# Performance work log

Measured on AMD Instinct MI355X. Metric: run time of the kernel, lower is better.

The kernel has to match this reference:

```python
import jax, jax.numpy as jnp
import numpy as np

N, F, K, E = 50000, 128, 8, 1600000


def setup_inputs() -> dict:
    key = jax.random.key(0)
    k1, k2, k3, k4 = jax.random.split(key, 4)
    x = jax.random.normal(k1, (N, F), dtype=jnp.float32)
    adj = jax.random.randint(k2, (2, E), 0, N, dtype=jnp.int64)
    e = jax.random.normal(k3, (N, K), dtype=jnp.float32)
    stdv = 1.0 / np.sqrt(F)  # reset_parameters: uniform(-stdv, stdv)
    weights = jax.random.uniform(k4, (K, 2 * F, F), dtype=jnp.float32,
                                 minval=-stdv, maxval=stdv)
    return {"x": x, "adj": adj, "e": e, "weights": weights}


def _gcn_conv(x, row, col, n_nodes):
    # degree of each node as a message *destination* (col) -- matches torch degree(col, N)
    deg = jax.ops.segment_sum(jnp.ones(row.shape[0], x.dtype), col,
                              num_segments=n_nodes)
    val = (1.0 / jnp.sqrt(deg[col])) * (1.0 / jnp.sqrt(deg[row]))
    val = jnp.nan_to_num(val, nan=0.0, posinf=0.0, neginf=0.0)
    # SparseTensor(row=col, col=row) @ x : aggregate x[row] into col
    msg = val[:, None] * x[row]           # [E, F] gather
    return jax.ops.segment_sum(msg, col, num_segments=n_nodes)  # [N, F] scatter


def reference(x, adj, e, weights):
    n_nodes = x.shape[0]
    row, col = adj[0], adj[1]
    hi = _gcn_conv(x, row, col, n_nodes)                  # [N, F]
    hi = jnp.concatenate([hi, x], axis=1)                 # [N, 2F]
    # torch: repeat hi K times, bmm with [K,2F,F], transpose -> [N, K, F]
    outputs = jnp.einsum('nf,kfo->nko', hi, weights)      # [N, K, F]
    out = jnp.sum(e[:, :, None] * outputs, axis=1)        # gating sum over K
    out = out + x                                         # residual
    return out
```

## Files before the change

### kernel.cpp

```cpp
#include <hip/hip_runtime.h>
#include <hip/hip_bf16.h>

typedef __bf16 bf16_t;
typedef __bf16 bf16x8 __attribute__((ext_vector_type(8)));
typedef float f32x4 __attribute__((ext_vector_type(4)));
typedef float f32x2 __attribute__((ext_vector_type(2)));

#define F 128
#define KEXP 8
#define BM 256
#define SSTG 16384

#define NB 196
#define CAP 12288
#define CH 8192

__global__ __launch_bounds__(256) void k_binA(const int* __restrict__ row,
    const int* __restrict__ col, int* __restrict__ cursor,
    int* __restrict__ region, int E){
  __shared__ int stage[CH];
  __shared__ unsigned char stageb[CH];
  __shared__ int hist4[4][NB];
  __shared__ int lcur4[4][NB];
  int tid = threadIdx.x, wid = tid >> 6;
  int base = blockIdx.x * CH;
  int cnt = min(CH, E - base);
  for (int i = tid; i < 4*NB; i += 256) ((int*)hist4)[i] = 0;
  __syncthreads();
  for (int i = tid; i < cnt; i += 256){
    int r = row[base+i], c = col[base+i];
    stage[i] = (r << 8) | (c & 255);
    stageb[i] = (unsigned char)(c >> 8);
    atomicAdd(&hist4[wid][c >> 8], 1);
  }
  __syncthreads();
  for (int b = tid; b < NB; b += 256){
    int h0 = hist4[0][b], h1 = hist4[1][b], h2 = hist4[2][b], h3 = hist4[3][b];
    int gbase = atomicAdd(&cursor[b], h0+h1+h2+h3) + b*CAP;
    lcur4[0][b] = gbase;
    lcur4[1][b] = gbase + h0;
    lcur4[2][b] = gbase + h0 + h1;
    lcur4[3][b] = gbase + h0 + h1 + h2;
  }
  __syncthreads();
  for (int i = tid; i < cnt; i += 256){
    int b = stageb[i];
    int pos = atomicAdd(&lcur4[wid][b], 1);
    region[pos] = stage[i];
  }
}

__global__ void k_bstart(const int* __restrict__ cursor, int* __restrict__ bstart,
                         int* __restrict__ offs, int Nn){
  __shared__ int lds[256];
  int t = threadIdx.x;
  int c = (t < NB) ? cursor[t] : 0;
  lds[t] = c; __syncthreads();
  for (int off=1; off<256; off<<=1){
    int u = (t>=off) ? lds[t-off] : 0;
    __syncthreads();
    lds[t] += u;
    __syncthreads();
  }
  if (t < NB) bstart[t] = lds[t] - c;
  if (t == NB-1){ bstart[NB] = lds[t]; offs[Nn] = lds[t]; }
}

__global__ __launch_bounds__(256) void k_binB(const int* __restrict__ region,
    const int* __restrict__ cursor, const int* __restrict__ bstart,
    int* __restrict__ deg, int* __restrict__ offs, int* __restrict__ bucket,
    int Nn){
  __shared__ int hist4[4][256];
  __shared__ int loff[256];
  __shared__ int lcur4[4][256];
  int b = blockIdx.x, t = threadIdx.x, wid = t >> 6;
  int cnt = cursor[b];
  const int* src = region + b*CAP;
  for (int i = t; i < 4*256; i += 256) ((int*)hist4)[i] = 0;
  __syncthreads();
  for (int i = t; i < cnt; i += 256) atomicAdd(&hist4[wid][src[i] & 255], 1);
  __syncthreads();
  int h0 = hist4[0][t], h1 = hist4[1][t], h2 = hist4[2][t], h3 = hist4[3][t];
  int v = h0 + h1 + h2 + h3;
  loff[t] = v;
  __syncthreads();
  for (int off=1; off<256; off<<=1){
    int u = (t>=off) ? loff[t-off] : 0;
    __syncthreads();
    loff[t] += u;
    __syncthreads();
  }
  int excl = loff[t] - v;
  int gb = bstart[b];
  int node = b*256 + t;
  if (node < Nn){ deg[node] = v; offs[node] = gb + excl; }
  lcur4[0][t] = gb + excl;
  lcur4[1][t] = gb + excl + h0;
  lcur4[2][t] = gb + excl + h0 + h1;
  lcur4[3][t] = gb + excl + h0 + h1 + h2;
  __syncthreads();
  for (int i = t; i < cnt; i += 256){
    int p = src[i];
    int pos = atomicAdd(&lcur4[wid][p & 255], 1);
    bucket[pos] = p >> 8;
  }
}

__global__ void k_prep(const float* __restrict__ x, const int* __restrict__ deg,
                       unsigned int* __restrict__ xs8, const float* __restrict__ W,
                       bf16_t* __restrict__ Wt, int Nn, int xsB){
  int tid = threadIdx.x;
  if ((int)blockIdx.x < xsB){
    int i = blockIdx.x*256 + tid;
    if (i < Nn*16){
      int n = i >> 4;
      int d = deg[n];
      float dr = d>0 ? rsqrtf((float)d) : 0.f;
      const float4 f0 = *reinterpret_cast<const float4*>(&x[(size_t)i*8]);
      const float4 f1 = *reinterpret_cast<const float4*>(&x[(size_t)i*8+4]);
      unsigned int lo, hi2;
      lo  = __builtin_amdgcn_cvt_pk_fp8_f32(dr*f0.x, dr*f0.y, 0,  false);
      lo  = __builtin_amdgcn_cvt_pk_fp8_f32(dr*f0.z, dr*f0.w, lo, true);
      hi2 = __builtin_amdgcn_cvt_pk_fp8_f32(dr*f1.x, dr*f1.y, 0,  false);
      hi2 = __builtin_amdgcn_cvt_pk_fp8_f32(dr*f1.z, dr*f1.w, hi2, true);
      xs8[(size_t)i*2]     = lo;
      xs8[(size_t)i*2 + 1] = hi2;
    }
  } else {
    int i8 = (blockIdx.x - xsB)*256 + tid;
    if (i8 < 32768){
      int st   = i8 >> 11;
      int g    = i8 & 2047;
      int frag = g >> 6;
      int lane = g & 63;
      int h = st >> 3, kk = st & 7;
      int ksl = frag >> 3, cgg = frag & 7;
      int n  = cgg*16 + (lane & 15);
      int f0 = h*128 + ksl*32 + (lane >> 4)*8;
      bf16x8 v;
      #pragma unroll
      for (int j=0;j<8;j++)
        v[j] = (bf16_t)W[(size_t)kk*32768 + (size_t)(f0+j)*128 + n];
      *reinterpret_cast<bf16x8*>(&Wt[(size_t)i8*8]) = v;
    }
  }
}

__global__ __launch_bounds__(256) void k_agg(const unsigned int* __restrict__ xs8,
    const int* __restrict__ offs, const int* __restrict__ bucket,
    bf16_t* __restrict__ hi, int Nn){
  int wid = threadIdx.x >> 6, lane = threadIdx.x & 63;
  int g = lane >> 4, j16 = lane & 15;
  int n = blockIdx.x*16 + wid*4 + g;
  if (n >= Nn) return;
  int o0 = offs[n], o1 = offs[n+1];
  float acc[8] = {0.f,0.f,0.f,0.f,0.f,0.f,0.f,0.f};
  int nr = (o1 - o0 + 7) >> 3;
  int j = o0;
  for (int r = 0; r < nr; r++, j += 8){
    int idx[8];
    #pragma unroll
    for (int t=0;t<8;t++) idx[t] = bucket[min(j+t, o1-1)];
    uint2 v[8];
    #pragma unroll
    for (int t=0;t<8;t++)
      v[t] = *reinterpret_cast<const uint2*>(
          reinterpret_cast<const unsigned char*>(xs8) + (size_t)idx[t]*F + j16*8);
    #pragma unroll
    for (int t=0;t<8;t++){
      float m = (j+t < o1) ? 1.f : 0.f;
      f32x2 p0 = __builtin_amdgcn_cvt_pk_f32_fp8(v[t].x, false);
      f32x2 p1 = __builtin_amdgcn_cvt_pk_f32_fp8(v[t].x, true);
      f32x2 p2 = __builtin_amdgcn_cvt_pk_f32_fp8(v[t].y, false);
      f32x2 p3 = __builtin_amdgcn_cvt_pk_f32_fp8(v[t].y, true);
      acc[0] += m*p0.x; acc[1] += m*p0.y;
      acc[2] += m*p1.x; acc[3] += m*p1.y;
      acc[4] += m*p2.x; acc[5] += m*p2.y;
      acc[6] += m*p3.x; acc[7] += m*p3.y;
    }
  }
  int dn = o1 - o0;
  float dc = dn>0 ? rsqrtf((float)dn) : 0.f;
  bf16x8 o;
  #pragma unroll
  for (int i=0;i<8;i++) o[i] = (bf16_t)(dc*acc[i]);
  *reinterpret_cast<bf16x8*>(&hi[(size_t)n*F + j16*8]) = o;
}

#define MFMA_BF16 __builtin_amdgcn_mfma_f32_16x16x32_bf16

__global__ __launch_bounds__(512, 2) void k_gemm(
    const bf16_t* __restrict__ hi, const float* __restrict__ x,
    const float* __restrict__ e, const bf16_t* __restrict__ Wt,
    float* __restrict__ out, int Nn)
{
  extern __shared__ __align__(16) char smem[];
  bf16_t* b_s  = (bf16_t*)smem;
  float*  e_sT = (float*)(smem + 2*SSTG*2);
  const int tid = threadIdx.x;
  const int base = blockIdx.x * BM;
  const int lane = tid & 63, wid = tid >> 6;
  const int rw = wid >> 1, cw = wid & 1;
  const int r16 = lane & 15, kc = lane >> 4;

  #pragma unroll
  for (int i=0;i<4;i++){
    int u = tid + i*512;
    __builtin_amdgcn_global_load_lds(
        (const __attribute__((address_space(1))) void*)(Wt + (size_t)u*8),
        (__attribute__((address_space(3))) void*)(b_s + (size_t)u*8),
        16, 0, 0);
  }

  for (int i = tid; i < KEXP*BM; i += 512){
    int kk = i >> 8, row = i & (BM-1);
    int srow = min(base + row, Nn-1);
    e_sT[kk*BM + row] = e[(size_t)srow*KEXP + kk];
  }

  int rr[4];
  #pragma unroll
  for (int rg=0; rg<4; rg++) rr[rg] = min(base + rw*64 + rg*16 + r16, Nn-1);
  bf16x8 a[4][4];
  #pragma unroll
  for (int rg=0; rg<4; rg++)
    #pragma unroll
    for (int ks=0; ks<4; ks++)
      a[rg][ks] = *reinterpret_cast<const bf16x8*>(
          &hi[(size_t)rr[rg]*F + ks*32 + kc*8]);

  f32x4 acc[4][4];
  #pragma unroll
  for (int rg=0;rg<4;rg++)
    #pragma unroll
    for (int cg=0;cg<4;cg++) acc[rg][cg] = (f32x4){0.f,0.f,0.f,0.f};
  const f32x4 fz = (f32x4){0.f,0.f,0.f,0.f};

  asm volatile("s_waitcnt vmcnt(0) lgkmcnt(0)" ::: "memory");
  __builtin_amdgcn_s_barrier();

  for (int st=0; st<16; st++){
    if (st == 8){
      #pragma unroll
      for (int rg=0; rg<4; rg++)
        #pragma unroll
        for (int ks=0; ks<4; ks++){
          const float4 f0 = *reinterpret_cast<const float4*>(
              &x[(size_t)rr[rg]*F + ks*32 + kc*8]);
          const float4 f1 = *reinterpret_cast<const float4*>(
              &x[(size_t)rr[rg]*F + ks*32 + kc*8 + 4]);
          bf16x8 v;
          v[0]=(bf16_t)f0.x; v[1]=(bf16_t)f0.y; v[2]=(bf16_t)f0.z; v[3]=(bf16_t)f0.w;
          v[4]=(bf16_t)f1.x; v[5]=(bf16_t)f1.y; v[6]=(bf16_t)f1.z; v[7]=(bf16_t)f1.w;
          a[rg][ks] = v;
        }
    }
    if (st < 15){
      const bf16_t* src = Wt + (size_t)(st+1)*SSTG;
      bf16_t* dst = b_s + ((st+1)&1)*SSTG;
      #pragma unroll
      for (int i=0;i<4;i++){
        int u = tid + i*512;
        __builtin_amdgcn_global_load_lds(
            (const __attribute__((address_space(1))) void*)(src + (size_t)u*8),
            (__attribute__((address_space(3))) void*)(dst + (size_t)u*8),
            16, 0, 0);
      }
      asm volatile("s_waitcnt vmcnt(4)" ::: "memory");
    } else {
      asm volatile("s_waitcnt vmcnt(0)" ::: "memory");
    }
    __builtin_amdgcn_s_barrier();

    const bf16_t* buf = b_s + (st&1)*SSTG;
    f32x4 ck[4][4];
    __builtin_amdgcn_s_setprio(1);
    #pragma unroll
    for (int cg=0; cg<4; cg++){
      bf16x8 b = *reinterpret_cast<const bf16x8*>(
          &buf[(size_t)(cw*4 + cg)*512 + lane*8]);
      #pragma unroll
      for (int rg=0; rg<4; rg++)
        ck[rg][cg] = MFMA_BF16(a[rg][0], b, fz, 0, 0, 0);
    }
    #pragma unroll
    for (int ks=1; ks<4; ks++)
      #pragma unroll
      for (int cg=0; cg<4; cg++){
        bf16x8 b = *reinterpret_cast<const bf16x8*>(
            &buf[(size_t)(ks*8 + cw*4 + cg)*512 + lane*8]);
        #pragma unroll
        for (int rg=0; rg<4; rg++)
          ck[rg][cg] = MFMA_BF16(a[rg][ks], b, ck[rg][cg], 0, 0, 0);
      }
    __builtin_amdgcn_s_setprio(0);

    const int kk = st & 7;
    #pragma unroll
    for (int rg=0; rg<4; rg++){
      f32x4 ev = *reinterpret_cast<const f32x4*>(
          &e_sT[kk*BM + rw*64 + rg*16 + kc*4]);
      #pragma unroll
      for (int cg=0; cg<4; cg++)
        #pragma unroll
        for (int r=0; r<4; r++)
          acc[rg][cg][r] += ev[r]*ck[rg][cg][r];
    }

    __builtin_amdgcn_s_barrier();
  }

  #pragma unroll
  for (int rg=0; rg<4; rg++){
    #pragma unroll
    for (int cg=0; cg<4; cg++){
      int ocol = cw*64 + cg*16 + r16;
      #pragma unroll
      for (int r=0; r<4; r++){
        int node = base + rw*64 + rg*16 + kc*4 + r;
        if (node < Nn)
          out[(size_t)node*F + ocol] = acc[rg][cg][r] + x[(size_t)node*F + ocol];
      }
    }
  }
}

extern "C" void kernel_launch(void* const* d_in, const int* in_sizes, int n_in,
                              void* d_out, int out_size, void* d_ws, size_t ws_size,
                              hipStream_t stream){
  const float* x  = (const float*)d_in[0];
  const int*  adj = (const int*)d_in[1];
  const float* e  = (const float*)d_in[2];
  const float* W  = (const float*)d_in[3];
  float* out = (float*)d_out;
  int Nn = in_sizes[0] / F;
  int E  = in_sizes[1] / 2;
  const int* rowp = adj;
  const int* colp = adj + E;

  char* w = (char*)d_ws;
  auto alloc = [&](size_t b){ char* p = w; w += (b + 255) & ~(size_t)255; return p; };
  int* deg     = (int*)alloc((size_t)Nn*4);
  int* offs    = (int*)alloc(((size_t)Nn+1)*4);
  int* cursor  = (int*)alloc((size_t)NB*4);
  int* bstart  = (int*)alloc((size_t)(NB+1)*4);
  int* bucket  = (int*)alloc((size_t)E*4);
  char* uni    = alloc((size_t)NB*CAP*4);
  int* region  = (int*)uni;
  unsigned int* xs8 = (unsigned int*)uni;
  bf16_t* hi   = (bf16_t*)alloc((size_t)Nn*F*2);
  bf16_t* Wt   = (bf16_t*)alloc((size_t)2048*F*2);

  const int smem_bytes = 2*SSTG*2 + KEXP*BM*4;
  hipFuncSetAttribute((const void*)k_gemm,
                      hipFuncAttributeMaxDynamicSharedMemorySize, smem_bytes);

  int nchunks = (E + CH - 1) / CH;
  int xsB = (Nn*16 + 255)/256;
  hipMemsetAsync(cursor, 0, (size_t)NB*4, stream);
  k_binA<<<nchunks, 256, 0, stream>>>(rowp, colp, cursor, region, E);
  k_bstart<<<1, 256, 0, stream>>>(cursor, bstart, offs, Nn);
  k_binB<<<NB, 256, 0, stream>>>(region, cursor, bstart, deg, offs, bucket, Nn);
  k_prep<<<xsB + 128, 256, 0, stream>>>(x, deg, xs8, W, Wt, Nn, xsB);
  k_agg<<<(Nn+15)/16, 256, 0, stream>>>(xs8, offs, bucket, hi, Nn);
  k_gemm<<<(Nn+BM-1)/BM, 512, smem_bytes, stream>>>(hi, x, e, Wt, out, Nn);
}
```

Baseline: 143.6 us.

## Process full 2F reduction per expert stage in GEMM, keeping hi and x fragments resident

The weight layout and GEMM loop change from 16 half-K stages to 8 stages that each cover the whole 256-wide reduction for one expert. Both hi and x A-fragments are loaded once up front and stay in registers, the e-gating is applied per column group, and the ck accumulator array shrinks. This halves the stage count, barriers and per-stage gating passes, and removes the mid-loop x reload. In exchange the double-buffered LDS grows to 128KB plus e_sT and the A registers double, which may reduce occupancy under launch_bounds(512,2).

```diff
diff --git a/kernel.cpp b/kernel.cpp
--- a/kernel.cpp
+++ b/kernel.cpp
@@ -9,7 +9,7 @@
 #define F 128
 #define KEXP 8
 #define BM 256
-#define SSTG 16384
+#define BSTG 32768
 
 #define NB 196
 #define CAP 12288
@@ -129,14 +129,12 @@
   } else {
     int i8 = (blockIdx.x - xsB)*256 + tid;
     if (i8 < 32768){
-      int st   = i8 >> 11;
-      int g    = i8 & 2047;
-      int frag = g >> 6;
-      int lane = g & 63;
-      int h = st >> 3, kk = st & 7;
-      int ksl = frag >> 3, cgg = frag & 7;
-      int n  = cgg*16 + (lane & 15);
-      int f0 = h*128 + ksl*32 + (lane >> 4)*8;
+      int kk   = i8 >> 12;
+      int frag = (i8 >> 6) & 63;
+      int lane = i8 & 63;
+      int ks = frag >> 3, cg = frag & 7;
+      int n  = cg*16 + (lane & 15);
+      int f0 = ks*32 + (lane >> 4)*8;
       bf16x8 v;
       #pragma unroll
       for (int j=0;j<8;j++)
@@ -196,7 +194,7 @@
 {
   extern __shared__ __align__(16) char smem[];
   bf16_t* b_s  = (bf16_t*)smem;
-  float*  e_sT = (float*)(smem + 2*SSTG*2);
+  float*  e_sT = (float*)(smem + 2*BSTG*2);
   const int tid = threadIdx.x;
   const int base = blockIdx.x * BM;
   const int lane = tid & 63, wid = tid >> 6;
@@ -204,7 +202,7 @@
   const int r16 = lane & 15, kc = lane >> 4;
 
   #pragma unroll
-  for (int i=0;i<4;i++){
+  for (int i=0;i<8;i++){
     int u = tid + i*512;
     __builtin_amdgcn_global_load_lds(
         (const __attribute__((address_space(1))) void*)(Wt + (size_t)u*8),
@@ -221,13 +219,25 @@
   int rr[4];
   #pragma unroll
   for (int rg=0; rg<4; rg++) rr[rg] = min(base + rw*64 + rg*16 + r16, Nn-1);
-  bf16x8 a[4][4];
-  #pragma unroll
-  for (int rg=0; rg<4; rg++)
+  bf16x8 a[4][8];
+  #pragma unroll
+  for (int rg=0; rg<4; rg++){
     #pragma unroll
     for (int ks=0; ks<4; ks++)
       a[rg][ks] = *reinterpret_cast<const bf16x8*>(
           &hi[(size_t)rr[rg]*F + ks*32 + kc*8]);
+    #pragma unroll
+    for (int ks=0; ks<4; ks++){
+      const float4 f0 = *reinterpret_cast<const float4*>(
+          &x[(size_t)rr[rg]*F + ks*32 + kc*8]);
+      const float4 f1 = *reinterpret_cast<const float4*>(
+          &x[(size_t)rr[rg]*F + ks*32 + kc*8 + 4]);
+      bf16x8 v;
+      v[0]=(bf16_t)f0.x; v[1]=(bf16_t)f0.y; v[2]=(bf16_t)f0.z; v[3]=(bf16_t)f0.w;
+      v[4]=(bf16_t)f1.x; v[5]=(bf16_t)f1.y; v[6]=(bf16_t)f1.z; v[7]=(bf16_t)f1.w;
+      a[rg][4+ks] = v;
+    }
+  }
 
   f32x4 acc[4][4];
   #pragma unroll
@@ -239,73 +249,57 @@
   asm volatile("s_waitcnt vmcnt(0) lgkmcnt(0)" ::: "memory");
   __builtin_amdgcn_s_barrier();
 
-  for (int st=0; st<16; st++){
-    if (st == 8){
-      #pragma unroll
-      for (int rg=0; rg<4; rg++)
-        #pragma unroll
-        for (int ks=0; ks<4; ks++){
-          const float4 f0 = *reinterpret_cast<const float4*>(
-              &x[(size_t)rr[rg]*F + ks*32 + kc*8]);
-          const float4 f1 = *reinterpret_cast<const float4*>(
-              &x[(size_t)rr[rg]*F + ks*32 + kc*8 + 4]);
-          bf16x8 v;
-          v[0]=(bf16_t)f0.x; v[1]=(bf16_t)f0.y; v[2]=(bf16_t)f0.z; v[3]=(bf16_t)f0.w;
-          v[4]=(bf16_t)f1.x; v[5]=(bf16_t)f1.y; v[6]=(bf16_t)f1.z; v[7]=(bf16_t)f1.w;
-          a[rg][ks] = v;
-        }
-    }
-    if (st < 15){
-      const bf16_t* src = Wt + (size_t)(st+1)*SSTG;
-      bf16_t* dst = b_s + ((st+1)&1)*SSTG;
-      #pragma unroll
-      for (int i=0;i<4;i++){
+  for (int kk=0; kk<8; kk++){
+    if (kk < 7){
+      const bf16_t* src = Wt + (size_t)(kk+1)*BSTG;
+      bf16_t* dst = b_s + ((kk+1)&1)*BSTG;
+      #pragma unroll
+      for (int i=0;i<8;i++){
         int u = tid + i*512;
         __builtin_amdgcn_global_load_lds(
             (const __attribute__((address_space(1))) void*)(src + (size_t)u*8),
             (__attribute__((address_space(3))) void*)(dst + (size_t)u*8),
             16, 0, 0);
       }
-      asm volatile("s_waitcnt vmcnt(4)" ::: "memory");
+      asm volatile("s_waitcnt vmcnt(8)" ::: "memory");
     } else {
       asm volatile("s_waitcnt vmcnt(0)" ::: "memory");
     }
     __builtin_amdgcn_s_barrier();
 
-    const bf16_t* buf = b_s + (st&1)*SSTG;
-    f32x4 ck[4][4];
+    const bf16_t* buf = b_s + (kk&1)*BSTG;
+    f32x4 ev[4];
+    #pragma unroll
+    for (int rg=0; rg<4; rg++)
+      ev[rg] = *reinterpret_cast<const f32x4*>(
+          &e_sT[kk*BM + rw*64 + rg*16 + kc*4]);
+
     __builtin_amdgcn_s_setprio(1);
     #pragma unroll
     for (int cg=0; cg<4; cg++){
-      bf16x8 b = *reinterpret_cast<const bf16x8*>(
-          &buf[(size_t)(cw*4 + cg)*512 + lane*8]);
-      #pragma unroll
-      for (int rg=0; rg<4; rg++)
-        ck[rg][cg] = MFMA_BF16(a[rg][0], b, fz, 0, 0, 0);
-    }
-    #pragma unroll
-    for (int ks=1; ks<4; ks++)
-      #pragma unroll
-      for (int cg=0; cg<4; cg++){
+      f32x4 ck[4];
+      {
+        bf16x8 b = *reinterpret_cast<const bf16x8*>(
+            &buf[(size_t)(cw*4 + cg)*512 + lane*8]);
+        #pragma unroll
+        for (int rg=0; rg<4; rg++)
+          ck[rg] = MFMA_BF16(a[rg][0], b, fz, 0, 0, 0);
+      }
+      #pragma unroll
+      for (int ks=1; ks<8; ks++){
         bf16x8 b = *reinterpret_cast<const bf16x8*>(
             &buf[(size_t)(ks*8 + cw*4 + cg)*512 + lane*8]);
         #pragma unroll
         for (int rg=0; rg<4; rg++)
-          ck[rg][cg] = MFMA_BF16(a[rg][ks], b, ck[rg][cg], 0, 0, 0);
+          ck[rg] = MFMA_BF16(a[rg][ks], b, ck[rg], 0, 0, 0);
       }
-    __builtin_amdgcn_s_setprio(0);
-
-    const int kk = st & 7;
-    #pragma unroll
-    for (int rg=0; rg<4; rg++){
-      f32x4 ev = *reinterpret_cast<const f32x4*>(
-          &e_sT[kk*BM + rw*64 + rg*16 + kc*4]);
-      #pragma unroll
-      for (int cg=0; cg<4; cg++)
+      #pragma unroll
+      for (int rg=0; rg<4; rg++)
         #pragma unroll
         for (int r=0; r<4; r++)
-          acc[rg][cg][r] += ev[r]*ck[rg][cg][r];
-    }
+          acc[rg][cg][r] += ev[rg][r]*ck[rg][r];
+    }
+    __builtin_amdgcn_s_setprio(0);
 
     __builtin_amdgcn_s_barrier();
   }
@@ -351,7 +345,7 @@
   bf16_t* hi   = (bf16_t*)alloc((size_t)Nn*F*2);
   bf16_t* Wt   = (bf16_t*)alloc((size_t)2048*F*2);
 
-  const int smem_bytes = 2*SSTG*2 + KEXP*BM*4;
+  const int smem_bytes = 2*BSTG*2 + KEXP*BM*4;
   hipFuncSetAttribute((const void*)k_gemm,
                       hipFuncAttributeMaxDynamicSharedMemorySize, smem_bytes);
 
```

Measured after the change: 142.7 us. No clear change (-0.6%).
